# Optimization experiments

Hardware: AMD Instinct MI355X
Metric: run time of the kernel (lower is better)

Reference implementation:

```python
import jax, jax.numpy as jnp
import numpy as np
import math

# Model config (matches init_kwargs)
V, D, H, L, DFF, S_MAX = 32000, 512, 8, 6, 2048, 1024
DK = D // H


def _layernorm(x, g, b, eps=1e-5):
    m = jnp.mean(x, axis=-1, keepdims=True)
    v = jnp.mean(jnp.square(x - m), axis=-1, keepdims=True)
    return (x - m) / jnp.sqrt(v + eps) * g + b


def _pos_encoding(seq_len, d_model):
    # sin on even dims, cos on odd dims
    pos = jnp.arange(seq_len, dtype=jnp.float32)[:, None]          # [S,1]
    div = jnp.exp(jnp.arange(0, d_model, 2, dtype=jnp.float32) *
                  (-math.log(10000.0) / d_model))                   # [D/2]
    ang = pos * div                                                 # [S,D/2]
    pe = jnp.stack([jnp.sin(ang), jnp.cos(ang)], axis=-1)           # [S,D/2,2]
    return pe.reshape(seq_len, d_model)                             # [S,D]


def setup_inputs() -> dict:
    key = jax.random.key(0)
    ks = jax.random.split(key, 24)
    sd = 0.02

    def n(k, shape):
        return jax.random.normal(k, shape, jnp.float32) * sd

    B, S = 2, 1024
    return {
        "tokens": jax.random.randint(ks[0], (B, S), 0, V, dtype=jnp.int32),
        "tok_emb": n(ks[1], (V, D)),
        # attention projections, [L, D, D] stored as (in, out)
        "Wq": n(ks[2], (L, D, D)), "bq": jnp.zeros((L, D)),
        "Wk": n(ks[3], (L, D, D)), "bk": jnp.zeros((L, D)),
        "Wv": n(ks[4], (L, D, D)), "bv": jnp.zeros((L, D)),
        "Wo": n(ks[5], (L, D, D)), "bo": jnp.zeros((L, D)),
        "ln1_g": jnp.ones((L, D)), "ln1_b": jnp.zeros((L, D)),
        "W1": n(ks[6], (L, D, DFF)), "b1": jnp.zeros((L, DFF)),
        "W2": n(ks[7], (L, DFF, D)), "b2": jnp.zeros((L, D)),
        "ln2_g": jnp.ones((L, D)), "ln2_b": jnp.zeros((L, D)),
        "lnf_g": jnp.ones((D,)), "lnf_b": jnp.zeros((D,)),
        "Wout": n(ks[8], (D, V)), "bout": jnp.zeros((V,)),
    }


def reference(tokens, tok_emb, Wq, bq, Wk, bk, Wv, bv, Wo, bo,
              ln1_g, ln1_b, W1, b1, W2, b2, ln2_g, ln2_b,
              lnf_g, lnf_b, Wout, bout):
    B, S = tokens.shape
    x = tok_emb[tokens] * math.sqrt(D) + _pos_encoding(S, D)[None]   # [B,S,D]
    causal = jnp.tril(jnp.ones((S, S), dtype=bool))[None, None]       # [1,1,S,S]
    scale = math.sqrt(DK)

    attns = []
    for l in range(L):
        q = (x @ Wq[l] + bq[l]).reshape(B, S, H, DK).transpose(0, 2, 1, 3)
        k = (x @ Wk[l] + bk[l]).reshape(B, S, H, DK).transpose(0, 2, 1, 3)
        v = (x @ Wv[l] + bv[l]).reshape(B, S, H, DK).transpose(0, 2, 1, 3)
        scores = jnp.einsum('bhsk,bhtk->bhst', q, k) / scale           # [B,H,S,S]
        scores = jnp.where(causal, scores, -1e9)
        a = jax.nn.softmax(scores, axis=-1)
        ctx = jnp.einsum('bhst,bhtk->bhsk', a, v)                      # [B,H,S,DK]
        ctx = ctx.transpose(0, 2, 1, 3).reshape(B, S, D)
        attn_out = ctx @ Wo[l] + bo[l]
        x = _layernorm(x + attn_out, ln1_g[l], ln1_b[l])
        h = jax.nn.gelu(x @ W1[l] + b1[l], approximate=False)          # torch GELU (exact)
        ff = h @ W2[l] + b2[l]
        x = _layernorm(x + ff, ln2_g[l], ln2_b[l])
        attns.append(a)

    x = _layernorm(x, lnf_g, lnf_b)
    logits = x @ Wout + bout                                           # [B,S,V]
    return logits, jnp.stack(attns)                                    # attn: [L,B,H,S,S]
```

## Files before the change

kernel.cpp:

```cpp
#include <hip/hip_runtime.h>
#include <math.h>

#define NB 2
#define NS 1024
#define NH 8
#define NDK 64
#define ND 512
#define NDFF 2048
#define NV 32000
#define NL 6
#define MROWS (NB * NS)
#define QKVLD (3 * ND)

using bf16_t = __bf16;
using bf16x4 = __attribute__((ext_vector_type(4))) __bf16;
using bf16x8 = __attribute__((ext_vector_type(8))) __bf16;
using f32x4  = __attribute__((ext_vector_type(4))) float;

__device__ __forceinline__ void gload_lds16(const bf16_t* g, bf16_t* l) {
  __builtin_amdgcn_global_load_lds(
      (const __attribute__((address_space(1))) void*)g,
      (__attribute__((address_space(3))) void*)l, 16, 0, 0);
}

__device__ __forceinline__ float gelu_exact(float v) {
  return 0.5f * v * (1.0f + erff(v * 0.7071067811865476f));
}

__global__ __launch_bounds__(256)
void prep_kernel(const int* __restrict__ tokens, const float* __restrict__ emb,
                 const float* __restrict__ Wq, const float* __restrict__ Wk,
                 const float* __restrict__ Wv, const float* __restrict__ Wo,
                 const float* __restrict__ W1, const float* __restrict__ W2,
                 const float* __restrict__ Wout,
                 bf16_t* __restrict__ WqkvT, bf16_t* __restrict__ WoT,
                 bf16_t* __restrict__ W1T, bf16_t* __restrict__ W2T,
                 bf16_t* __restrict__ WoutT,
                 float* __restrict__ x, bf16_t* __restrict__ xb) {
  __shared__ bf16_t T[64][72];
  const int id = blockIdx.x;
  const int tid = threadIdx.x;

  if (id >= 8608) {
    const int row = id - 8608;
    const int s = row & (NS - 1);
    const int tok = tokens[row];
    const float SQRTD = 22.627416997969522f;
    const float C = -9.210340371976184f / (float)ND;
#pragma unroll
    for (int i = 0; i < 2; ++i) {
      const int d = tid + i * 256;
      const int pair = d >> 1;
      const float div = expf((float)(2 * pair) * C);
      const float ang = (float)s * div;
      const float pe = (d & 1) ? cosf(ang) : sinf(ang);
      const float v = emb[(size_t)tok * ND + d] * SQRTD + pe;
      x[(size_t)row * ND + d] = v;
      xb[(size_t)row * ND + d] = (bf16_t)v;
    }
    return;
  }

  const float* src; bf16_t* dst; int K, N, n0, k0;
  if (id < 1536) {
    const int z = id >> 6, t = id & 63;
    const int mat = z / 6, layer = z % 6;
    src = ((mat == 0) ? Wq : (mat == 1) ? Wk : (mat == 2) ? Wv : Wo) + (size_t)layer * ND * ND;
    dst = (mat < 3) ? (WqkvT + (size_t)layer * QKVLD * ND + (size_t)mat * ND * ND)
                    : (WoT + (size_t)layer * ND * ND);
    K = ND; N = ND; n0 = (t & 7) * 64; k0 = (t >> 3) * 64;
  } else if (id < 3072) {
    const int idx = id - 1536, layer = idx >> 8, t = idx & 255;
    src = W1 + (size_t)layer * ND * NDFF; dst = W1T + (size_t)layer * NDFF * ND;
    K = ND; N = NDFF; n0 = (t & 31) * 64; k0 = (t >> 5) * 64;
  } else if (id < 4608) {
    const int idx = id - 3072, layer = idx >> 8, t = idx & 255;
    src = W2 + (size_t)layer * NDFF * ND; dst = W2T + (size_t)layer * ND * NDFF;
    K = NDFF; N = ND; n0 = (t & 7) * 64; k0 = (t >> 3) * 64;
  } else {
    const int t = id - 4608;
    src = Wout; dst = WoutT;
    K = ND; N = NV; n0 = (t % 500) * 64; k0 = (t / 500) * 64;
  }

#pragma unroll
  for (int it = 0; it < 4; ++it) {
    const int k = (tid >> 4) + it * 16;
    const int c = (tid & 15) * 4;
    const float4 v = *(const float4*)&src[(size_t)(k0 + k) * N + n0 + c];
    T[c + 0][k] = (bf16_t)v.x;
    T[c + 1][k] = (bf16_t)v.y;
    T[c + 2][k] = (bf16_t)v.z;
    T[c + 3][k] = (bf16_t)v.w;
  }
  __syncthreads();
  const int n = tid >> 2, kk = (tid & 3) * 16;
  bf16x8 a = *(const bf16x8*)&T[n][kk];
  bf16x8 b2v = *(const bf16x8*)&T[n][kk + 8];
  *(bf16x8*)&dst[(size_t)(n0 + n) * K + k0 + kk] = a;
  *(bf16x8*)&dst[(size_t)(n0 + n) * K + k0 + kk + 8] = b2v;
}

__global__ __launch_bounds__(256)
void add_ln_kernel(float* __restrict__ x, const float* __restrict__ y0,
                   const float* __restrict__ y1,
                   const float* __restrict__ g, const float* __restrict__ bb,
                   bf16_t* __restrict__ xb) {
  const int row = blockIdx.x, tid = threadIdx.x;
  const size_t base = (size_t)row * ND;
  float v0 = x[base + tid], v1 = x[base + tid + 256];
  if (y0) { v0 += y0[base + tid]; v1 += y0[base + tid + 256]; }
  if (y1) { v0 += y1[base + tid]; v1 += y1[base + tid + 256]; }
  __shared__ float red[256];
  red[tid] = v0 + v1; __syncthreads();
  for (int o = 128; o > 0; o >>= 1) {
    if (tid < o) red[tid] += red[tid + o];
    __syncthreads();
  }
  const float mean = red[0] * (1.f / (float)ND);
  __syncthreads();
  const float d0 = v0 - mean, d1 = v1 - mean;
  red[tid] = d0 * d0 + d1 * d1; __syncthreads();
  for (int o = 128; o > 0; o >>= 1) {
    if (tid < o) red[tid] += red[tid + o];
    __syncthreads();
  }
  const float inv = 1.f / sqrtf(red[0] * (1.f / (float)ND) + 1e-5f);
  const float o0 = d0 * inv * g[tid]       + bb[tid];
  const float o1 = d1 * inv * g[tid + 256] + bb[tid + 256];
  x[base + tid] = o0;
  x[base + tid + 256] = o1;
  xb[base + tid] = (bf16_t)o0; xb[base + tid + 256] = (bf16_t)o1;
}

template <int ACT, int OUTBF>
__global__ __launch_bounds__(256)
void gemm_bt(const bf16_t* __restrict__ A, const bf16_t* __restrict__ Wt,
             const float* __restrict__ B0,
             void* __restrict__ Cout, int N, int K, int lda, int ldc) {
  __shared__ bf16_t As[128 * 64];
  __shared__ bf16_t Bs[128 * 64];
  const int tid = threadIdx.x, lane = tid & 63, w = tid >> 6;
  const int wm = w >> 1, wn = w & 1;
  const int lcol = lane & 15, hi = lane >> 4;

  const int nwg = gridDim.x * gridDim.y;
  const int flat = blockIdx.y * gridDim.x + blockIdx.x;
  const int q = nwg >> 3, r = nwg & 7;
  const int xcd = flat & 7, idx = flat >> 3;
  const int nf = (xcd < r ? xcd * (q + 1) : r * (q + 1) + (xcd - r) * q) + idx;
  const int m0 = (nf % gridDim.x) * 128, n0 = (nf / gridDim.x) * 128;

  const int sr8 = lane >> 3;
  const int sslot = lane & 7;

  f32x4 acc[4][4] = {};

  for (int k0 = 0; k0 < K; k0 += 64) {
#pragma unroll
    for (int t = 0; t < 2; ++t) {
#pragma unroll
      for (int c = 0; c < 2; ++c) {
        const int rbase = t * 64 + w * 16 + c * 8;
        const int row = rbase + sr8;
        const int ks = sslot ^ (row & 7);
        gload_lds16(&A[(size_t)(m0 + row) * lda + k0 + ks * 8], &As[rbase * 64]);
        gload_lds16(&Wt[(size_t)(n0 + row) * K + k0 + ks * 8], &Bs[rbase * 64]);
      }
    }
    __syncthreads();

#pragma unroll
    for (int kk = 0; kk < 2; ++kk) {
      bf16x8 af[4], bf[4];
#pragma unroll
      for (int m = 0; m < 4; ++m) {
        const int rr = wm * 64 + m * 16 + lcol;
        af[m] = *(const bf16x8*)&As[rr * 64 + (((kk * 4 + hi) ^ (rr & 7)) * 8)];
      }
#pragma unroll
      for (int n = 0; n < 4; ++n) {
        const int rr = wn * 64 + n * 16 + lcol;
        bf[n] = *(const bf16x8*)&Bs[rr * 64 + (((kk * 4 + hi) ^ (rr & 7)) * 8)];
      }
#pragma unroll
      for (int m = 0; m < 4; ++m)
#pragma unroll
        for (int n = 0; n < 4; ++n)
          acc[m][n] = __builtin_amdgcn_mfma_f32_16x16x32_bf16(bf[n], af[m], acc[m][n], 0, 0, 0);
    }
    __syncthreads();
  }

#pragma unroll
  for (int m = 0; m < 4; ++m) {
    const int row = m0 + wm * 64 + m * 16 + lcol;
#pragma unroll
    for (int n = 0; n < 4; ++n) {
      const int col = n0 + wn * 64 + n * 16 + hi * 4;
      const f32x4 bv = *(const f32x4*)&B0[col];
      f32x4 v;
#pragma unroll
      for (int i = 0; i < 4; ++i) {
        float t = acc[m][n][i] + bv[i];
        if (ACT == 1) t = gelu_exact(t);
        v[i] = t;
      }
      if (OUTBF) {
        bf16x4 o;
#pragma unroll
        for (int i = 0; i < 4; ++i) o[i] = (bf16_t)v[i];
        *(bf16x4*)&((bf16_t*)Cout)[(size_t)row * ldc + col] = o;
      } else {
        __builtin_nontemporal_store(v, (f32x4*)&((float*)Cout)[(size_t)row * ldc + col]);
      }
    }
  }
}

__global__ __launch_bounds__(256)
void gemm_qkv64(const bf16_t* __restrict__ A, const bf16_t* __restrict__ Wt,
                const float* __restrict__ B0, const float* __restrict__ B1,
                const float* __restrict__ B2,
                bf16_t* __restrict__ Cout, int K, int lda, int ldc) {
  __shared__ bf16_t As[64 * 128];
  __shared__ bf16_t Bs[64 * 128];
  const int tid = threadIdx.x, lane = tid & 63, w = tid >> 6;
  const int wm = w >> 1, wn = w & 1;
  const int lcol = lane & 15, hi = lane >> 4;
  const int m0 = blockIdx.x * 64, n0 = blockIdx.y * 64;
  const int sr4 = lane >> 4, sslot = lane & 15;

  f32x4 acc[2][2] = {};

  for (int k0 = 0; k0 < K; k0 += 128) {
#pragma unroll
    for (int c = 0; c < 4; ++c) {
      const int rbase = w * 16 + c * 4;
      const int row = rbase + sr4;
      const int ks = sslot ^ (row & 15);
      gload_lds16(&A[(size_t)(m0 + row) * lda + k0 + ks * 8], &As[rbase * 128]);
      gload_lds16(&Wt[(size_t)(n0 + row) * K + k0 + ks * 8], &Bs[rbase * 128]);
    }
    __syncthreads();

#pragma unroll
    for (int kk = 0; kk < 4; ++kk) {
      bf16x8 af[2], bf[2];
#pragma unroll
      for (int m = 0; m < 2; ++m) {
        const int rr = wm * 32 + m * 16 + lcol;
        af[m] = *(const bf16x8*)&As[rr * 128 + (((kk * 4 + hi) ^ (rr & 15)) * 8)];
      }
#pragma unroll
      for (int n = 0; n < 2; ++n) {
        const int rr = wn * 32 + n * 16 + lcol;
        bf[n] = *(const bf16x8*)&Bs[rr * 128 + (((kk * 4 + hi) ^ (rr & 15)) * 8)];
      }
#pragma unroll
      for (int m = 0; m < 2; ++m)
#pragma unroll
        for (int n = 0; n < 2; ++n)
          acc[m][n] = __builtin_amdgcn_mfma_f32_16x16x32_bf16(bf[n], af[m], acc[m][n], 0, 0, 0);
    }
    __syncthreads();
  }

#pragma unroll
  for (int m = 0; m < 2; ++m) {
    const int row = m0 + wm * 32 + m * 16 + lcol;
#pragma unroll
    for (int n = 0; n < 2; ++n) {
      const int col = n0 + wn * 32 + n * 16 + hi * 4;
      const int sel = col >> 9;
      const float* Bp = (sel == 0) ? B0 : (sel == 1) ? B1 : B2;
      const f32x4 bv = *(const f32x4*)&Bp[col & 511];
      bf16x4 o;
#pragma unroll
      for (int i = 0; i < 4; ++i) o[i] = (bf16_t)(acc[m][n][i] + bv[i]);
      *(bf16x4*)&Cout[(size_t)row * ldc + col] = o;
    }
  }
}

template <int ACT, int OUTBF>
__global__ __launch_bounds__(256)
void gemm64(const bf16_t* __restrict__ A, const bf16_t* __restrict__ Wt,
            const float* __restrict__ bias,
            void* __restrict__ Cout, int K, int lda, int ldc, size_t zstride) {
  __shared__ bf16_t As[64 * 128];
  __shared__ bf16_t Bs[64 * 128];
  const int tid = threadIdx.x, lane = tid & 63, w = tid >> 6;
  const int wm = w >> 1, wn = w & 1;
  const int lcol = lane & 15, hi = lane >> 4;
  const int m0 = blockIdx.x * 64, n0 = blockIdx.y * 64;
  const int sr4 = lane >> 4, sslot = lane & 15;
  const int kc = K / gridDim.z;
  const int kbeg = blockIdx.z * kc;

  f32x4 acc[2][2] = {};

  for (int k0 = kbeg; k0 < kbeg + kc; k0 += 128) {
#pragma unroll
    for (int c = 0; c < 4; ++c) {
      const int rbase = w * 16 + c * 4;
      const int row = rbase + sr4;
      const int ks = sslot ^ (row & 15);
      gload_lds16(&A[(size_t)(m0 + row) * lda + k0 + ks * 8], &As[rbase * 128]);
      gload_lds16(&Wt[(size_t)(n0 + row) * K + k0 + ks * 8], &Bs[rbase * 128]);
    }
    __syncthreads();

#pragma unroll
    for (int kk = 0; kk < 4; ++kk) {
      bf16x8 af[2], bf[2];
#pragma unroll
      for (int m = 0; m < 2; ++m) {
        const int rr = wm * 32 + m * 16 + lcol;
        af[m] = *(const bf16x8*)&As[rr * 128 + (((kk * 4 + hi) ^ (rr & 15)) * 8)];
      }
#pragma unroll
      for (int n = 0; n < 2; ++n) {
        const int rr = wn * 32 + n * 16 + lcol;
        bf[n] = *(const bf16x8*)&Bs[rr * 128 + (((kk * 4 + hi) ^ (rr & 15)) * 8)];
      }
#pragma unroll
      for (int m = 0; m < 2; ++m)
#pragma unroll
        for (int n = 0; n < 2; ++n)
          acc[m][n] = __builtin_amdgcn_mfma_f32_16x16x32_bf16(bf[n], af[m], acc[m][n], 0, 0, 0);
    }
    __syncthreads();
  }

#pragma unroll
  for (int m = 0; m < 2; ++m) {
    const int row = m0 + wm * 32 + m * 16 + lcol;
#pragma unroll
    for (int n = 0; n < 2; ++n) {
      const int col = n0 + wn * 32 + n * 16 + hi * 4;
      f32x4 bv = {0.f, 0.f, 0.f, 0.f};
      if (blockIdx.z == 0) bv = *(const f32x4*)&bias[col];
      f32x4 v;
#pragma unroll
      for (int i = 0; i < 4; ++i) {
        float t = acc[m][n][i] + bv[i];
        if (ACT == 1) t = gelu_exact(t);
        v[i] = t;
      }
      if (OUTBF) {
        bf16x4 o;
#pragma unroll
        for (int i = 0; i < 4; ++i) o[i] = (bf16_t)v[i];
        *(bf16x4*)&((bf16_t*)Cout)[(size_t)row * ldc + col] = o;
      } else {
        *(f32x4*)&((float*)Cout)[blockIdx.z * zstride + (size_t)row * ldc + col] = v;
      }
    }
  }
}

__global__ __launch_bounds__(256)
void attn_fused(const bf16_t* __restrict__ qkv, float* __restrict__ probs,
                bf16_t* __restrict__ ctx) {
  const int qt = 15 - blockIdx.x;
  const int h = blockIdx.y, b = blockIdx.z;
  const int q0 = qt * 64;
  const int NTT = (q0 >> 7) + 1;
  const int qmax = q0 + 63;
  const int tid = threadIdx.x, lane = tid & 63, wq = tid >> 6;
  const int lcol = lane & 15, hi = lane >> 4;

  __shared__ bf16_t Qs[64][72];
  __shared__ bf16_t Ks[128][72];
  __shared__ bf16_t Vs[64][132];
  __shared__ bf16_t Ps[64][132];

  {
    const int r = tid >> 2, c = (tid & 3) * 16;
    const bf16_t* src = &qkv[((size_t)(b * NS + q0 + r)) * QKVLD + h * NDK + c];
    *(bf16x8*)&Qs[r][c]     = *(const bf16x8*)&src[0];
    *(bf16x8*)&Qs[r][c + 8] = *(const bf16x8*)&src[8];
  }
  __syncthreads();
  const bf16x8 qf0 = *(const bf16x8*)&Qs[wq * 16 + lcol][hi * 8];
  const bf16x8 qf1 = *(const bf16x8*)&Qs[wq * 16 + lcol][32 + hi * 8];
  const int qrow = q0 + wq * 16 + lcol;
  const float scale = 0.125f;

  float m_run = -1e30f, s_run = 0.f;

  for (int tt = 0; tt < NTT; ++tt) {
    const int t0 = tt * 128;
    const int fmax = min(8, ((qmax - t0) >> 4) + 1);
    {
      const int r = tid >> 1, cb = (tid & 1) * 32;
      const bf16_t* src = &qkv[((size_t)(b * NS + t0 + r)) * QKVLD + ND + h * NDK + cb];
#pragma unroll
      for (int j = 0; j < 4; ++j)
        *(bf16x8*)&Ks[r][cb + j * 8] = *(const bf16x8*)&src[j * 8];
    }
    __syncthreads();

    float tmax = -1e30f;
    f32x4 sc[8];
#pragma unroll
    for (int f = 0; f < 8; ++f) {
      if (f >= fmax) break;
      f32x4 s4 = {};
      const bf16x8 ka0 = *(const bf16x8*)&Ks[f * 16 + lcol][hi * 8];
      const bf16x8 ka1 = *(const bf16x8*)&Ks[f * 16 + lcol][32 + hi * 8];
      s4 = __builtin_amdgcn_mfma_f32_16x16x32_bf16(ka0, qf0, s4, 0, 0, 0);
      s4 = __builtin_amdgcn_mfma_f32_16x16x32_bf16(ka1, qf1, s4, 0, 0, 0);
#pragma unroll
      for (int i = 0; i < 4; ++i) {
        const int t = t0 + f * 16 + hi * 4 + i;
        const float v = (t <= qrow) ? s4[i] * scale : -1e30f;
        s4[i] = v;
        tmax = fmaxf(tmax, v);
      }
      sc[f] = s4;
    }
    tmax = fmaxf(tmax, __shfl_xor(tmax, 16));
    tmax = fmaxf(tmax, __shfl_xor(tmax, 32));
    const float m_new = fmaxf(m_run, tmax);
    float sum = 0.f;
#pragma unroll
    for (int f = 0; f < 8; ++f) {
      if (f >= fmax) break;
#pragma unroll
      for (int i = 0; i < 4; ++i) sum += __expf(sc[f][i] - m_new);
    }
    sum += __shfl_xor(sum, 16);
    sum += __shfl_xor(sum, 32);
    s_run = s_run * __expf(m_run - m_new) + sum;
    m_run = m_new;
    __syncthreads();
  }
  const float inv = 1.f / s_run;

  f32x4 cacc[4] = {};
  const size_t prow = (((size_t)b * NH + h) * NS + qrow) * NS;
  for (int tt = NTT - 1; tt >= 0; --tt) {
    const int t0 = tt * 128;
    const int fmax = min(8, ((qmax - t0) >> 4) + 1);
    if (tt != NTT - 1) {
      const int r = tid >> 1, cb = (tid & 1) * 32;
      const bf16_t* src = &qkv[((size_t)(b * NS + t0 + r)) * QKVLD + ND + h * NDK + cb];
#pragma unroll
      for (int j = 0; j < 4; ++j)
        *(bf16x8*)&Ks[r][cb + j * 8] = *(const bf16x8*)&src[j * 8];
    }
    {
#pragma unroll
      for (int it = 0; it < 2; ++it) {
        const int t4 = (tid >> 4) * 4 + it * 64;
        const int dk4 = (tid & 15) * 4;
        bf16x4 rr[4];
#pragma unroll
        for (int i = 0; i < 4; ++i)
          rr[i] = *(const bf16x4*)&qkv[((size_t)(b * NS + t0 + t4 + i)) * QKVLD + 2 * ND + h * NDK + dk4];
#pragma unroll
        for (int j = 0; j < 4; ++j) {
          bf16x4 c;
#pragma unroll
          for (int i = 0; i < 4; ++i) c[i] = rr[i][j];
          *(bf16x4*)&Vs[dk4 + j][t4] = c;
        }
      }
    }
    __syncthreads();

    const f32x4 zf = {0.f, 0.f, 0.f, 0.f};
    const bf16x4 zb = {(bf16_t)0.f, (bf16_t)0.f, (bf16_t)0.f, (bf16_t)0.f};
#pragma unroll
    for (int f = 0; f < 8; ++f) {
      if (f < fmax) {
        f32x4 s4 = {};
        const bf16x8 ka0 = *(const bf16x8*)&Ks[f * 16 + lcol][hi * 8];
        const bf16x8 ka1 = *(const bf16x8*)&Ks[f * 16 + lcol][32 + hi * 8];
        s4 = __builtin_amdgcn_mfma_f32_16x16x32_bf16(ka0, qf0, s4, 0, 0, 0);
        s4 = __builtin_amdgcn_mfma_f32_16x16x32_bf16(ka1, qf1, s4, 0, 0, 0);
        f32x4 pw;
        bf16x4 pb;
#pragma unroll
        for (int i = 0; i < 4; ++i) {
          const int t = t0 + f * 16 + hi * 4 + i;
          const float v = (t <= qrow) ? s4[i] * scale : -1e30f;
          const float p = __expf(v - m_run) * inv;
          pw[i] = p;
          pb[i] = (bf16_t)p;
        }
        __builtin_nontemporal_store(pw, (f32x4*)&probs[prow + t0 + f * 16 + hi * 4]);
        *(bf16x4*)&Ps[wq * 16 + lcol][f * 16 + hi * 4] = pb;
      } else {
        __builtin_nontemporal_store(zf, (f32x4*)&probs[prow + t0 + f * 16 + hi * 4]);
        *(bf16x4*)&Ps[wq * 16 + lcol][f * 16 + hi * 4] = zb;
      }
    }

#pragma unroll
    for (int ks = 0; ks < 4; ++ks) {
      const bf16x8 pf = *(const bf16x8*)&Ps[wq * 16 + lcol][ks * 32 + hi * 8];
#pragma unroll
      for (int df = 0; df < 4; ++df) {
        const bf16x8 vf = *(const bf16x8*)&Vs[df * 16 + lcol][ks * 32 + hi * 8];
        cacc[df] = __builtin_amdgcn_mfma_f32_16x16x32_bf16(vf, pf, cacc[df], 0, 0, 0);
      }
    }
    __syncthreads();
  }

#pragma unroll
  for (int df = 0; df < 4; ++df) {
    bf16x4 o;
#pragma unroll
    for (int i = 0; i < 4; ++i) o[i] = (bf16_t)cacc[df][i];
    *(bf16x4*)&ctx[((size_t)(b * NS + q0 + wq * 16 + lcol)) * ND + h * NDK + df * 16 + hi * 4] = o;
  }

  const int z0 = NTT * 128;
  const int nz = (NS - z0) >> 2;
  if (nz > 0) {
    const f32x4 zf = {0.f, 0.f, 0.f, 0.f};
    for (int idx = tid; idx < 64 * nz; idx += 256) {
      const int r = idx / nz, c = (idx - r * nz) * 4;
      __builtin_nontemporal_store(zf,
          (f32x4*)&probs[(((size_t)b * NH + h) * NS + q0 + r) * NS + z0 + c]);
    }
  }
}

extern "C" void kernel_launch(void* const* d_in, const int* in_sizes, int n_in,
                              void* d_out, int out_size, void* d_ws, size_t ws_size,
                              hipStream_t stream) {
  const int*   tokens  = (const int*)d_in[0];
  const float* tok_emb = (const float*)d_in[1];
  const float* Wq = (const float*)d_in[2];
  const float* bq = (const float*)d_in[3];
  const float* Wk = (const float*)d_in[4];
  const float* bk = (const float*)d_in[5];
  const float* Wv = (const float*)d_in[6];
  const float* bv = (const float*)d_in[7];
  const float* Wo = (const float*)d_in[8];
  const float* bo = (const float*)d_in[9];
  const float* ln1_g = (const float*)d_in[10];
  const float* ln1_b = (const float*)d_in[11];
  const float* W1 = (const float*)d_in[12];
  const float* b1 = (const float*)d_in[13];
  const float* W2 = (const float*)d_in[14];
  const float* b2 = (const float*)d_in[15];
  const float* ln2_g = (const float*)d_in[16];
  const float* ln2_b = (const float*)d_in[17];
  const float* lnf_g = (const float*)d_in[18];
  const float* lnf_b = (const float*)d_in[19];
  const float* Wout = (const float*)d_in[20];
  const float* bout = (const float*)d_in[21];

  float* logits   = (float*)d_out;
  float* attn_all = (float*)d_out + (size_t)NB * NS * NV;

  char* w = (char*)d_ws;
  float* x    = (float*)w;  w += (size_t)4 << 20;
  float* tmp  = (float*)w;  w += (size_t)8 << 20;
  bf16_t* xb  = (bf16_t*)w; w += (size_t)2 << 20;
  bf16_t* qkv = (bf16_t*)w; w += (size_t)6 << 20;
  bf16_t* ctx = (bf16_t*)w; w += (size_t)2 << 20;
  bf16_t* hh  = (bf16_t*)w; w += (size_t)8 << 20;
  bf16_t* WqkvT = (bf16_t*)w; w += (size_t)6 * QKVLD * ND * 2;
  bf16_t* WoT   = (bf16_t*)w; w += (size_t)6 * ND * ND * 2;
  bf16_t* W1T   = (bf16_t*)w; w += (size_t)6 * NDFF * ND * 2;
  bf16_t* W2T   = (bf16_t*)w; w += (size_t)6 * ND * NDFF * 2;
  bf16_t* WoutT = (bf16_t*)w; w += (size_t)NV * ND * 2;
  if ((size_t)(w - (char*)d_ws) > ws_size) return;

  const int M = MROWS;
  const size_t U = (size_t)M * ND;
  float* tmp1 = tmp + U;

  prep_kernel<<<10656, 256, 0, stream>>>(tokens, tok_emb, Wq, Wk, Wv, Wo, W1, W2, Wout,
                                         WqkvT, WoT, W1T, W2T, WoutT, x, xb);

  const dim3 gQKV(M / 64, QKVLD / 64);
  const dim3 gFF1(M / 64, NDFF / 64);
  const dim3 gOut(M / 128, NV / 128);
  const dim3 g64s(M / 64, ND / 64, 2);
  const dim3 gAttn(16, NH, NB);

  for (int l = 0; l < NL; ++l) {
    gemm_qkv64<<<gQKV, 256, 0, stream>>>(xb, WqkvT + (size_t)l * QKVLD * ND,
        bq + l * ND, bk + l * ND, bv + l * ND, qkv, ND, ND, QKVLD);

    float* probs_l = attn_all + (size_t)l * NB * NH * NS * NS;
    attn_fused<<<gAttn, 256, 0, stream>>>(qkv, probs_l, ctx);

    gemm64<0, 0><<<g64s, 256, 0, stream>>>(ctx, WoT + (size_t)l * ND * ND,
        bo + l * ND, tmp, ND, ND, ND, U);
    add_ln_kernel<<<M, 256, 0, stream>>>(x, tmp, tmp1, ln1_g + l * ND, ln1_b + l * ND, xb);

    gemm64<1, 1><<<gFF1, 256, 0, stream>>>(xb, W1T + (size_t)l * NDFF * ND,
        b1 + l * NDFF, hh, ND, ND, NDFF, 0);
    gemm64<0, 0><<<g64s, 256, 0, stream>>>(hh, W2T + (size_t)l * ND * NDFF,
        b2 + l * ND, tmp, NDFF, NDFF, ND, U);
    add_ln_kernel<<<M, 256, 0, stream>>>(x, tmp, tmp1, ln2_g + l * ND, ln2_b + l * ND, xb);
  }

  add_ln_kernel<<<M, 256, 0, stream>>>(x, nullptr, nullptr, lnf_g, lnf_b, xb);

  gemm_bt<0, 0><<<gOut, 256, 0, stream>>>(xb, WoutT, bout,
      logits, NV, ND, ND, NV);
}
```

Baseline: 684.6 us.

## Fuse final layernorm into last add_ln and read K directly from global in attention

Adds an optional second layernorm to add_ln_kernel so the final LN runs inside the last layer's add+LN, dropping one launch and one pass over x. In attention, the K tile is no longer staged through shared memory: each lane loads its MFMA K fragments straight from global memory, which removes the K-tile barriers and LDS traffic but issues more scattered, possibly redundant global reads. The second pass now walks tiles forward with rearranged barriers. The zero-fill of the masked probability region is moved to the kernel start so it overlaps with compute.

```diff
diff --git a/kernel.cpp b/kernel.cpp
--- a/kernel.cpp
+++ b/kernel.cpp
@@ -105,6 +105,7 @@
 void add_ln_kernel(float* __restrict__ x, const float* __restrict__ y0,
                    const float* __restrict__ y1,
                    const float* __restrict__ g, const float* __restrict__ bb,
+                   const float* __restrict__ g2, const float* __restrict__ bb2,
                    bf16_t* __restrict__ xb) {
   const int row = blockIdx.x, tid = threadIdx.x;
   const size_t base = (size_t)row * ND;
@@ -126,10 +127,31 @@
     __syncthreads();
   }
   const float inv = 1.f / sqrtf(red[0] * (1.f / (float)ND) + 1e-5f);
-  const float o0 = d0 * inv * g[tid]       + bb[tid];
-  const float o1 = d1 * inv * g[tid + 256] + bb[tid + 256];
-  x[base + tid] = o0;
-  x[base + tid + 256] = o1;
+  float o0 = d0 * inv * g[tid]       + bb[tid];
+  float o1 = d1 * inv * g[tid + 256] + bb[tid + 256];
+
+  if (g2) {
+    __syncthreads();
+    red[tid] = o0 + o1; __syncthreads();
+    for (int o = 128; o > 0; o >>= 1) {
+      if (tid < o) red[tid] += red[tid + o];
+      __syncthreads();
+    }
+    const float mean2 = red[0] * (1.f / (float)ND);
+    __syncthreads();
+    const float e0 = o0 - mean2, e1 = o1 - mean2;
+    red[tid] = e0 * e0 + e1 * e1; __syncthreads();
+    for (int o = 128; o > 0; o >>= 1) {
+      if (tid < o) red[tid] += red[tid + o];
+      __syncthreads();
+    }
+    const float inv2 = 1.f / sqrtf(red[0] * (1.f / (float)ND) + 1e-5f);
+    o0 = e0 * inv2 * g2[tid]       + bb2[tid];
+    o1 = e1 * inv2 * g2[tid + 256] + bb2[tid + 256];
+  } else {
+    x[base + tid] = o0;
+    x[base + tid + 256] = o1;
+  }
   xb[base + tid] = (bf16_t)o0; xb[base + tid + 256] = (bf16_t)o1;
 }
 
@@ -372,9 +394,21 @@
   const int lcol = lane & 15, hi = lane >> 4;
 
   __shared__ bf16_t Qs[64][72];
-  __shared__ bf16_t Ks[128][72];
   __shared__ bf16_t Vs[64][132];
   __shared__ bf16_t Ps[64][132];
+
+  {
+    const int z0 = NTT * 128;
+    const int nz = (NS - z0) >> 2;
+    if (nz > 0) {
+      const f32x4 zf = {0.f, 0.f, 0.f, 0.f};
+      for (int idx = tid; idx < 64 * nz; idx += 256) {
+        const int r = idx / nz, c = (idx - r * nz) * 4;
+        __builtin_nontemporal_store(zf,
+            (f32x4*)&probs[(((size_t)b * NH + h) * NS + q0 + r) * NS + z0 + c]);
+      }
+    }
+  }
 
   {
     const int r = tid >> 2, c = (tid & 3) * 16;
@@ -387,29 +421,22 @@
   const bf16x8 qf1 = *(const bf16x8*)&Qs[wq * 16 + lcol][32 + hi * 8];
   const int qrow = q0 + wq * 16 + lcol;
   const float scale = 0.125f;
+  const bf16_t* kbase = qkv + (size_t)b * NS * QKVLD + ND + h * NDK + hi * 8;
 
   float m_run = -1e30f, s_run = 0.f;
 
   for (int tt = 0; tt < NTT; ++tt) {
     const int t0 = tt * 128;
     const int fmax = min(8, ((qmax - t0) >> 4) + 1);
-    {
-      const int r = tid >> 1, cb = (tid & 1) * 32;
-      const bf16_t* src = &qkv[((size_t)(b * NS + t0 + r)) * QKVLD + ND + h * NDK + cb];
-#pragma unroll
-      for (int j = 0; j < 4; ++j)
-        *(bf16x8*)&Ks[r][cb + j * 8] = *(const bf16x8*)&src[j * 8];
-    }
-    __syncthreads();
-
     float tmax = -1e30f;
     f32x4 sc[8];
 #pragma unroll
     for (int f = 0; f < 8; ++f) {
       if (f >= fmax) break;
+      const bf16_t* kr = kbase + (size_t)(t0 + f * 16 + lcol) * QKVLD;
+      const bf16x8 ka0 = *(const bf16x8*)kr;
+      const bf16x8 ka1 = *(const bf16x8*)(kr + 32);
       f32x4 s4 = {};
-      const bf16x8 ka0 = *(const bf16x8*)&Ks[f * 16 + lcol][hi * 8];
-      const bf16x8 ka1 = *(const bf16x8*)&Ks[f * 16 + lcol][32 + hi * 8];
       s4 = __builtin_amdgcn_mfma_f32_16x16x32_bf16(ka0, qf0, s4, 0, 0, 0);
       s4 = __builtin_amdgcn_mfma_f32_16x16x32_bf16(ka1, qf1, s4, 0, 0, 0);
 #pragma unroll
@@ -435,22 +462,15 @@
     sum += __shfl_xor(sum, 32);
     s_run = s_run * __expf(m_run - m_new) + sum;
     m_run = m_new;
-    __syncthreads();
   }
   const float inv = 1.f / s_run;
 
   f32x4 cacc[4] = {};
   const size_t prow = (((size_t)b * NH + h) * NS + qrow) * NS;
-  for (int tt = NTT - 1; tt >= 0; --tt) {
+  for (int tt = 0; tt < NTT; ++tt) {
     const int t0 = tt * 128;
     const int fmax = min(8, ((qmax - t0) >> 4) + 1);
-    if (tt != NTT - 1) {
-      const int r = tid >> 1, cb = (tid & 1) * 32;
-      const bf16_t* src = &qkv[((size_t)(b * NS + t0 + r)) * QKVLD + ND + h * NDK + cb];
-#pragma unroll
-      for (int j = 0; j < 4; ++j)
-        *(bf16x8*)&Ks[r][cb + j * 8] = *(const bf16x8*)&src[j * 8];
-    }
+    __syncthreads();
     {
 #pragma unroll
       for (int it = 0; it < 2; ++it) {
@@ -469,16 +489,16 @@
         }
       }
     }
-    __syncthreads();
 
     const f32x4 zf = {0.f, 0.f, 0.f, 0.f};
     const bf16x4 zb = {(bf16_t)0.f, (bf16_t)0.f, (bf16_t)0.f, (bf16_t)0.f};
 #pragma unroll
     for (int f = 0; f < 8; ++f) {
       if (f < fmax) {
+        const bf16_t* kr = kbase + (size_t)(t0 + f * 16 + lcol) * QKVLD;
+        const bf16x8 ka0 = *(const bf16x8*)kr;
+        const bf16x8 ka1 = *(const bf16x8*)(kr + 32);
         f32x4 s4 = {};
-        const bf16x8 ka0 = *(const bf16x8*)&Ks[f * 16 + lcol][hi * 8];
-        const bf16x8 ka1 = *(const bf16x8*)&Ks[f * 16 + lcol][32 + hi * 8];
         s4 = __builtin_amdgcn_mfma_f32_16x16x32_bf16(ka0, qf0, s4, 0, 0, 0);
         s4 = __builtin_amdgcn_mfma_f32_16x16x32_bf16(ka1, qf1, s4, 0, 0, 0);
         f32x4 pw;
@@ -498,6 +518,7 @@
         *(bf16x4*)&Ps[wq * 16 + lcol][f * 16 + hi * 4] = zb;
       }
     }
+    __syncthreads();
 
 #pragma unroll
     for (int ks = 0; ks < 4; ++ks) {
@@ -508,7 +529,6 @@
         cacc[df] = __builtin_amdgcn_mfma_f32_16x16x32_bf16(vf, pf, cacc[df], 0, 0, 0);
       }
     }
-    __syncthreads();
   }
 
 #pragma unroll
@@ -517,17 +537,6 @@
 #pragma unroll
     for (int i = 0; i < 4; ++i) o[i] = (bf16_t)cacc[df][i];
     *(bf16x4*)&ctx[((size_t)(b * NS + q0 + wq * 16 + lcol)) * ND + h * NDK + df * 16 + hi * 4] = o;
-  }
-
-  const int z0 = NTT * 128;
-  const int nz = (NS - z0) >> 2;
-  if (nz > 0) {
-    const f32x4 zf = {0.f, 0.f, 0.f, 0.f};
-    for (int idx = tid; idx < 64 * nz; idx += 256) {
-      const int r = idx / nz, c = (idx - r * nz) * 4;
-      __builtin_nontemporal_store(zf,
-          (f32x4*)&probs[(((size_t)b * NH + h) * NS + q0 + r) * NS + z0 + c]);
-    }
   }
 }
 
@@ -596,16 +605,17 @@
 
     gemm64<0, 0><<<g64s, 256, 0, stream>>>(ctx, WoT + (size_t)l * ND * ND,
         bo + l * ND, tmp, ND, ND, ND, U);
-    add_ln_kernel<<<M, 256, 0, stream>>>(x, tmp, tmp1, ln1_g + l * ND, ln1_b + l * ND, xb);
+    add_ln_kernel<<<M, 256, 0, stream>>>(x, tmp, tmp1,
+        ln1_g + l * ND, ln1_b + l * ND, nullptr, nullptr, xb);
 
     gemm64<1, 1><<<gFF1, 256, 0, stream>>>(xb, W1T + (size_t)l * NDFF * ND,
         b1 + l * NDFF, hh, ND, ND, NDFF, 0);
     gemm64<0, 0><<<g64s, 256, 0, stream>>>(hh, W2T + (size_t)l * ND * NDFF,
         b2 + l * ND, tmp, NDFF, NDFF, ND, U);
-    add_ln_kernel<<<M, 256, 0, stream>>>(x, tmp, tmp1, ln2_g + l * ND, ln2_b + l * ND, xb);
-  }
-
-  add_ln_kernel<<<M, 256, 0, stream>>>(x, nullptr, nullptr, lnf_g, lnf_b, xb);
+    add_ln_kernel<<<M, 256, 0, stream>>>(x, tmp, tmp1,
+        ln2_g + l * ND, ln2_b + l * ND,
+        (l == NL - 1) ? lnf_g : nullptr, (l == NL - 1) ? lnf_b : nullptr, xb);
+  }
 
   gemm_bt<0, 0><<<gOut, 256, 0, stream>>>(xb, WoutT, bout,
       logits, NV, ND, ND, NV);
```

Result: slower. 806.9 us (+17.9%).
